# Performance work log

Hardware: AMD Instinct MI355X
Metric: run time of the kernel (lower is better)

## Reference

```python
import jax, jax.numpy as jnp
import numpy as np

B, P, S, D, L = 8, 64, 512, 512, 64


def setup_inputs() -> dict:
    key = jax.random.key(0)
    ks = jax.random.split(key, 12)
    span_repr = jax.random.normal(ks[0], (B, S, D), dtype=jnp.float32)
    predicates = jax.random.randint(ks[1], (B, P), 0, S, dtype=jnp.int64)
    labels = jax.random.randint(ks[2], (B, P, S), 0, L, dtype=jnp.int64)
    long_mask = jnp.ones((B, P, S), dtype=jnp.int64)
    sc = 1.0 / np.sqrt(D)
    # last-layer weights of FFNN linear_p / linear_a (only last layer matters in source)
    Wp = jax.random.normal(ks[3], (D, D), dtype=jnp.float32) * sc
    bp = jnp.zeros((D,), dtype=jnp.float32)
    Wa = jax.random.normal(ks[4], (D, D), dtype=jnp.float32) * sc
    ba = jnp.zeros((D,), dtype=jnp.float32)
    wp = jax.random.normal(ks[5], (D,), dtype=jnp.float32) * sc  # W_p (Linear D->1, no bias)
    wa = jax.random.normal(ks[6], (D,), dtype=jnp.float32) * sc  # W_a
    W1 = jax.random.normal(ks[7], (L, D, D), dtype=jnp.float32) * sc
    W2 = jax.random.normal(ks[8], (2 * D, L), dtype=jnp.float32) * sc
    b = jax.random.normal(ks[9], (1, L), dtype=jnp.float32) * 0.02
    return {"span_repr": span_repr, "predicates": predicates, "labels": labels,
            "long_mask": long_mask, "Wp": Wp, "bp": bp, "Wa": Wa, "ba": ba,
            "wp": wp, "wa": wa, "W1": W1, "W2": W2, "b": b}


def reference(span_repr, predicates, labels, long_mask, Wp, bp, Wa, ba, wp, wa, W1, W2, b):
    d = span_repr.shape[-1]
    # gather predicate representations: [B, P, D]
    pred_repr = jnp.take_along_axis(span_repr, predicates[..., None], axis=1)
    # FFNN (only last layer is effective in source) + scalar projections
    predicates_score = jax.nn.relu(pred_repr @ Wp.T + bp) @ wp        # [B, P]
    argument_score = jax.nn.relu(span_repr @ Wa.T + ba) @ wa          # [B, S]
    p_a_score = predicates_score[:, :, None] + argument_score[:, None, :]  # [B, P, S]
    # biaffine term: matmul(matmul(pred, W1), span^T) -> [B, P, S, L]
    first = jnp.einsum('bpd,lde,bse->bpsl', pred_repr, W1, span_repr)
    # concat(pred, span) @ W2, split to avoid materializing the concat
    second = (jnp.einsum('bpd,dl->bpl', pred_repr, W2[:d])[:, :, None, :]
              + jnp.einsum('bsd,dl->bsl', span_repr, W2[d:])[:, None, :, :])
    combine = first + second + b + p_a_score[..., None]               # [B, P, S, L]
    combine = combine.at[..., -1].set(0.0)
    num_labels = combine.shape[-1]
    # long_mask is all ones, so masked_select is the full flatten
    stack_instance = combine.reshape(-1, num_labels)                  # [B*P*S, L]
    stack_label = labels.reshape(-1)                                  # [B*P*S]
    return stack_instance, stack_label
```

## Files before the change

### kernel.cpp

```cpp
#include <hip/hip_runtime.h>
#include <hip/hip_bf16.h>

typedef __bf16 bf16x8 __attribute__((ext_vector_type(8)));
typedef float f32x4 __attribute__((ext_vector_type(4)));
typedef unsigned short ushort_t;

#define SS 512
#define DD 512
#define LL 64

__device__ __forceinline__ ushort_t f2b(float f) {
    union { float f; unsigned u; } x; x.f = f;
    unsigned r = x.u + 0x7FFFu + ((x.u >> 16) & 1u);
    return (ushort_t)(r >> 16);
}

__device__ __forceinline__ void async16(const void* g, void* l) {
    __builtin_amdgcn_global_load_lds(
        (const __attribute__((address_space(1))) unsigned int*)g,
        (__attribute__((address_space(3))) unsigned int*)l, 16, 0, 0);
}

__device__ __forceinline__ void stage_tile(const ushort_t* __restrict__ A, int lda,
                                           const ushort_t* __restrict__ Bt, int ldb,
                                           int k0, ushort_t* buf) {
    const int t = threadIdx.x;
    const int wbase = (t >> 6) << 10;
#pragma unroll
    for (int p = 0; p < 2; p++) {
        int row = (p << 7) + (t >> 2);
        int kg = (t & 3) ^ ((t >> 3) & 3);
        async16(A + (size_t)row * lda + k0 + kg * 8,
                (char*)buf + (p << 13) + wbase);
        async16(Bt + (size_t)row * ldb + k0 + kg * 8,
                (char*)(buf + 8192) + (p << 13) + wbase);
    }
}

__device__ __forceinline__ void gemm256(const ushort_t* __restrict__ A, int lda,
                                        const ushort_t* __restrict__ Bt, int ldb,
                                        ushort_t* lds, f32x4 (&acc)[8][4]) {
    const int t = threadIdx.x;
    const int lane = t & 63, wid = t >> 6;
    const int wm = wid >> 2, wn = wid & 3;
    const int r15 = lane & 15, kg = lane >> 4;
    const int sx = ((kg ^ ((r15 >> 1) & 3)) << 4);
    const f32x4 z4 = {0.f, 0.f, 0.f, 0.f};
#pragma unroll
    for (int i = 0; i < 8; i++)
#pragma unroll
        for (int j = 0; j < 4; j++) acc[i][j] = z4;

    stage_tile(A, lda, Bt, ldb, 0, lds);
    stage_tile(A, lda, Bt, ldb, 32, lds + 16384);

    for (int T = 0; T < 16; ++T) {
        if (T < 15) asm volatile("s_waitcnt vmcnt(4)" ::: "memory");
        else        asm volatile("s_waitcnt vmcnt(0)" ::: "memory");
        __builtin_amdgcn_s_barrier();
        __builtin_amdgcn_sched_barrier(0);
        const ushort_t* bufA = lds + (T % 3) * 16384;
        const ushort_t* bufB = bufA + 8192;
        const char* pa = (const char*)bufA + (wm * 128 + r15) * 64 + sx;
        const char* pb = (const char*)bufB + (wn * 64 + r15) * 64 + sx;
        bf16x8 af[8], bf[4];
#pragma unroll
        for (int mf = 0; mf < 8; mf++) af[mf] = *(const bf16x8*)(pa + mf * 1024);
#pragma unroll
        for (int nf = 0; nf < 4; nf++) bf[nf] = *(const bf16x8*)(pb + nf * 1024);
        if (T + 2 < 16)
            stage_tile(A, lda, Bt, ldb, (T + 2) * 32, lds + ((T + 2) % 3) * 16384);
#pragma unroll
        for (int mf = 0; mf < 8; mf++)
#pragma unroll
            for (int nf = 0; nf < 4; nf++)
                acc[mf][nf] = __builtin_amdgcn_mfma_f32_16x16x32_bf16(
                    af[mf], bf[nf], acc[mf][nf], 0, 0, 0);
    }
    __syncthreads();
}

__device__ __forceinline__ void stageA2(const ushort_t* __restrict__ A,
                                        int k0, ushort_t* buf) {
    const int t = threadIdx.x;
    const int wbase = (t >> 6) << 10;
#pragma unroll
    for (int p = 0; p < 2; p++) {
        int row = (p << 7) + (t >> 2);
        int kg = (t & 3) ^ ((t >> 3) & 3);
        async16(A + (size_t)row * DD + k0 + kg * 8, (char*)buf + (p << 13) + wbase);
    }
}

__device__ __forceinline__ void gemm256_w1(const ushort_t* __restrict__ predB,
                                           const float* __restrict__ W1le,
                                           ushort_t* lds, f32x4 (&acc)[8][4]) {
    const int t = threadIdx.x;
    const int lane = t & 63, wid = t >> 6;
    const int wm = wid >> 2, wn = wid & 3;
    const int r15 = lane & 15, kg = lane >> 4;
    const int sx = ((kg ^ ((r15 >> 1) & 3)) << 4);
    const f32x4 z4 = {0.f, 0.f, 0.f, 0.f};
#pragma unroll
    for (int i = 0; i < 8; i++)
#pragma unroll
        for (int j = 0; j < 4; j++) acc[i][j] = z4;

    const float* bbase = W1le + (size_t)(kg * 8) * DD + wn * 64 + r15;
    float fb[4][8];
    auto loadB = [&](int k0) {
#pragma unroll
        for (int nf = 0; nf < 4; nf++)
#pragma unroll
            for (int j = 0; j < 8; j++)
                fb[nf][j] = bbase[(size_t)(k0 + j) * DD + nf * 16];
    };

    loadB(0);
    stageA2(predB, 0, lds);
    stageA2(predB, 32, lds + 8192);

    for (int T = 0; T < 16; ++T) {
        if (T < 15) asm volatile("s_waitcnt vmcnt(2)" ::: "memory");
        else        asm volatile("s_waitcnt vmcnt(0)" ::: "memory");
        __builtin_amdgcn_s_barrier();
        __builtin_amdgcn_sched_barrier(0);
        bf16x8 bf[4];
#pragma unroll
        for (int nf = 0; nf < 4; nf++)
#pragma unroll
            for (int j = 0; j < 8; j++) bf[nf][j] = (__bf16)fb[nf][j];
        if (T + 1 < 16) loadB((T + 1) * 32);
        if (T + 2 < 16) stageA2(predB, (T + 2) * 32, lds + ((T + 2) % 3) * 8192);
        const char* pa = (const char*)(lds + (T % 3) * 8192)
                         + (wm * 128 + r15) * 64 + sx;
        bf16x8 af[8];
#pragma unroll
        for (int mf = 0; mf < 8; mf++) af[mf] = *(const bf16x8*)(pa + mf * 1024);
#pragma unroll
        for (int mf = 0; mf < 8; mf++)
#pragma unroll
            for (int nf = 0; nf < 4; nf++)
                acc[mf][nf] = __builtin_amdgcn_mfma_f32_16x16x32_bf16(
                    af[mf], bf[nf], acc[mf][nf], 0, 0, 0);
    }
    __syncthreads();
}

__global__ void __launch_bounds__(512, 2) k_U_small(
    const ushort_t* __restrict__ predB, const float* __restrict__ W1,
    ushort_t* __restrict__ UB,
    const ushort_t* __restrict__ spanB, const ushort_t* __restrict__ WaB,
    const ushort_t* __restrict__ WpB, const ushort_t* __restrict__ W2bT,
    const ushort_t* __restrict__ W2aT,
    const float* __restrict__ ba_, const float* __restrict__ bp_,
    const float* __restrict__ wa, const float* __restrict__ wp,
    float* ascore, float* pscore, float* spanW2, float* predW2) {
    extern __shared__ ushort_t lds[];
    const f32x4 z4 = {0.f, 0.f, 0.f, 0.f};
    const int t = threadIdx.x, lane = t & 63;
    const int r15 = lane & 15, kg = lane >> 4;
    if (blockIdx.x < 256) {
        f32x4 acc[8][4];
        int swz = (blockIdx.x & 7) * 32 + (blockIdx.x >> 3);
        int m0 = (swz & 1) * 256, n0 = (swz >> 1) * 256;
        int l = n0 >> 9, e0 = n0 & 511;
        gemm256_w1(predB + (size_t)m0 * DD, W1 + ((size_t)l * DD) * DD + e0, lds, acc);
        const int wid = t >> 6;
        const int wm = wid >> 2, wn = wid & 3;
        ushort_t* my = lds + wid * 4096;
        int gm = m0 + wm * 128, gn = n0 + wn * 64;
#pragma unroll
        for (int ch = 0; ch < 2; ch++) {
#pragma unroll
            for (int mf2 = 0; mf2 < 4; mf2++)
#pragma unroll
                for (int nf = 0; nf < 4; nf++)
#pragma unroll
                    for (int j = 0; j < 4; j++)
                        my[(mf2 * 16 + kg * 4 + j) * 64 + nf * 16 + r15] =
                            f2b(acc[ch * 4 + mf2][nf][j]);
#pragma unroll
            for (int it = 0; it < 8; it++) {
                int lr = it * 8 + (lane >> 3);
                bf16x8 v = *(const bf16x8*)(my + lr * 64 + (lane & 7) * 8);
                *(bf16x8*)(UB + (size_t)(gm + ch * 64 + lr) * 32768 + gn
                           + (lane & 7) * 8) = v;
            }
        }
        return;
    }
    const bool act = t < 256;
    ushort_t* As = lds;
    ushort_t* Bs = lds + 4096;
    const int wid4 = (t >> 6) & 3;
    const int o0 = wid4 * 1024 + lane * 16;
    int blk = blockIdx.x - 256;
    if (blk < 144) {
        const ushort_t *A, *Bt; const float *bias, *w; float* sc; int m0, n0;
        if (blk < 128) { A = spanB; Bt = WaB; bias = ba_; w = wa; sc = ascore;
                         m0 = (blk >> 2) * 128; n0 = (blk & 3) * 128; }
        else { int q = blk - 128; A = predB; Bt = WpB; bias = bp_; w = wp; sc = pscore;
               m0 = (q >> 2) * 128; n0 = (q & 3) * 128; }
        const ushort_t* Ab = A + (size_t)m0 * DD;
        const ushort_t* Bb = Bt + (size_t)n0 * DD;
        f32x4 acc[4][4];
#pragma unroll
        for (int i = 0; i < 4; i++)
#pragma unroll
            for (int j = 0; j < 4; j++) acc[i][j] = z4;
        int wr = (wid4 >> 1) * 64, wc = (wid4 & 1) * 64;
        for (int k0 = 0; k0 < DD; k0 += 32) {
            if (act) {
#pragma unroll
                for (int p = 0; p < 2; p++) {
                    int o = o0 + p * 4096;
                    async16(Ab + (size_t)(o >> 6) * DD + k0 + ((o & 63) >> 1), (char*)As + o);
                    async16(Bb + (size_t)(o >> 6) * DD + k0 + ((o & 63) >> 1), (char*)Bs + o);
                }
            }
            __syncthreads();
            if (act) {
                bf16x8 af[4], bf[4];
#pragma unroll
                for (int mf = 0; mf < 4; mf++)
                    af[mf] = *(const bf16x8*)(As + (wr + mf * 16 + r15) * 32 + kg * 8);
#pragma unroll
                for (int nf = 0; nf < 4; nf++)
                    bf[nf] = *(const bf16x8*)(Bs + (wc + nf * 16 + r15) * 32 + kg * 8);
#pragma unroll
                for (int mf = 0; mf < 4; mf++)
#pragma unroll
                    for (int nf = 0; nf < 4; nf++)
                        acc[mf][nf] = __builtin_amdgcn_mfma_f32_16x16x32_bf16(
                            af[mf], bf[nf], acc[mf][nf], 0, 0, 0);
            }
            __syncthreads();
        }
        if (act) {
#pragma unroll
            for (int mf = 0; mf < 4; mf++)
#pragma unroll
                for (int j = 0; j < 4; j++) {
                    float v = 0.f;
#pragma unroll
                    for (int nf = 0; nf < 4; nf++) {
                        int col = n0 + wc + nf * 16 + r15;
                        float c = acc[mf][nf][j] + bias[col];
                        if (c > 0.f) v += c * w[col];
                    }
                    v += __shfl_xor(v, 1); v += __shfl_xor(v, 2);
                    v += __shfl_xor(v, 4); v += __shfl_xor(v, 8);
                    if (r15 == 0) atomicAdd(&sc[m0 + wr + mf * 16 + kg * 4 + j], v);
                }
        }
    } else {
        int q = blk - 144;
        const ushort_t *A, *Bt; float* C; int m0;
        if (q < 32) { A = spanB; Bt = W2bT; C = spanW2; m0 = q * 128; }
        else { A = predB; Bt = W2aT; C = predW2; m0 = (q - 32) * 128; }
        const ushort_t* Ab = A + (size_t)m0 * DD;
        f32x4 acc[4][2];
#pragma unroll
        for (int i = 0; i < 4; i++) { acc[i][0] = z4; acc[i][1] = z4; }
        int wr = (wid4 >> 1) * 64, wc = (wid4 & 1) * 32;
        for (int k0 = 0; k0 < DD; k0 += 32) {
            if (act) {
#pragma unroll
                for (int p = 0; p < 2; p++) {
                    int o = o0 + p * 4096;
                    async16(Ab + (size_t)(o >> 6) * DD + k0 + ((o & 63) >> 1), (char*)As + o);
                }
                int o = o0;
                async16(Bt + (size_t)(o >> 6) * DD + k0 + ((o & 63) >> 1), (char*)Bs + o);
            }
            __syncthreads();
            if (act) {
                bf16x8 af[4], bf[2];
#pragma unroll
                for (int mf = 0; mf < 4; mf++)
                    af[mf] = *(const bf16x8*)(As + (wr + mf * 16 + r15) * 32 + kg * 8);
#pragma unroll
                for (int nf = 0; nf < 2; nf++)
                    bf[nf] = *(const bf16x8*)(Bs + (wc + nf * 16 + r15) * 32 + kg * 8);
#pragma unroll
                for (int mf = 0; mf < 4; mf++)
#pragma unroll
                    for (int nf = 0; nf < 2; nf++)
                        acc[mf][nf] = __builtin_amdgcn_mfma_f32_16x16x32_bf16(
                            af[mf], bf[nf], acc[mf][nf], 0, 0, 0);
            }
            __syncthreads();
        }
        if (act) {
#pragma unroll
            for (int mf = 0; mf < 4; mf++)
#pragma unroll
                for (int nf = 0; nf < 2; nf++)
#pragma unroll
                    for (int j = 0; j < 4; j++) {
                        int m = m0 + wr + mf * 16 + kg * 4 + j;
                        int n = wc + nf * 16 + r15;
                        C[(size_t)m * LL + n] = acc[mf][nf][j];
                    }
        }
    }
}

__global__ void __launch_bounds__(512, 2) k_out256(const ushort_t* __restrict__ spanB,
    const ushort_t* __restrict__ UB, const float* __restrict__ spanW2,
    const float* __restrict__ predW2, const float* __restrict__ ascore,
    const float* __restrict__ pscore, const float* __restrict__ bias,
    float* __restrict__ out) {
    extern __shared__ ushort_t lds[];
    f32x4 acc[8][4];
    int swz = (blockIdx.x & 7) * 32 + (blockIdx.x >> 3);
    int b = swz >> 5, r = swz & 31;
    int m0 = (r & 1) * 256, n0 = (r >> 1) * 256;
    gemm256(spanB + ((size_t)b * SS + m0) * DD, DD,
            UB + ((size_t)b * 4096 + n0) * DD, DD, lds, acc);
    const int t = threadIdx.x, lane = t & 63, wid = t >> 6;
    const int wm = wid >> 2, wn = wid & 3, r15 = lane & 15, kg = lane >> 4;
    float cn[4]; int nn[4];
#pragma unroll
    for (int nf = 0; nf < 4; nf++) {
        int n = n0 + wn * 64 + nf * 16 + r15;
        nn[nf] = n;
        cn[nf] = bias[n & 63] + predW2[b * 4096 + n] + pscore[b * 64 + (n >> 6)];
    }
#pragma unroll
    for (int mf = 0; mf < 8; mf++)
#pragma unroll
        for (int j = 0; j < 4; j++) {
            int s = m0 + wm * 128 + mf * 16 + kg * 4 + j;
            float as_ = ascore[b * SS + s];
            const float* sw = spanW2 + ((size_t)b * SS + s) * LL;
#pragma unroll
            for (int nf = 0; nf < 4; nf++) {
                int n = nn[nf], l = n & 63, p = n >> 6;
                float v = acc[mf][nf][j] + cn[nf] + as_ + sw[l];
                if (l == LL - 1) v = 0.f;
                out[(((size_t)b * 64 + p) * SS + s) * LL + l] = v;
            }
        }
}

__global__ __launch_bounds__(256) void k_prep(
    const float* __restrict__ span, const int* __restrict__ preds,
    const int* __restrict__ labels, const float* __restrict__ Wa,
    const float* __restrict__ Wp, const float* __restrict__ W2,
    ushort_t* spanB, ushort_t* predB, ushort_t* WaB, ushort_t* WpB,
    ushort_t* W2aT, ushort_t* W2bT, float* out, float* scores) {
    int blk = blockIdx.x;
    if (blk < 4096) {
        int id = blk * 256 + threadIdx.x;
        if (id < 524288) {
            float4 v = ((const float4*)span)[id];
            ((ushort4*)spanB)[id] = make_ushort4(f2b(v.x), f2b(v.y), f2b(v.z), f2b(v.w));
        } else if (id < 589824) {
            int j = id - 524288;
            int row = j >> 7, c4 = j & 127;
            int b = row >> 6;
            int idx = preds[row];
            float4 v = ((const float4*)(span + ((size_t)(b * SS + idx)) * DD))[c4];
            ((ushort4*)(predB + (size_t)row * DD))[c4] =
                make_ushort4(f2b(v.x), f2b(v.y), f2b(v.z), f2b(v.w));
        } else if (id < 851968) {
            int k = id - 589824;
            out[16777216 + k] = (float)labels[k];
        } else if (id < 917504) {
            int j = id - 851968;
            float4 v = ((const float4*)Wa)[j];
            ((ushort4*)WaB)[j] = make_ushort4(f2b(v.x), f2b(v.y), f2b(v.z), f2b(v.w));
        } else if (id < 983040) {
            int j = id - 917504;
            float4 v = ((const float4*)Wp)[j];
            ((ushort4*)WpB)[j] = make_ushort4(f2b(v.x), f2b(v.y), f2b(v.z), f2b(v.w));
        } else if (id < 1015808) {
            int j = id - 983040;
            W2aT[j] = f2b(W2[(size_t)(j & 511) * LL + (j >> 9)]);
        } else {
            int j = id - 1015808;
            W2bT[j] = f2b(W2[(size_t)((j & 511) + DD) * LL + (j >> 9)]);
        }
    } else {
        int idx = (blk - 4096) * 256 + threadIdx.x;
        if (idx < 4608) scores[idx] = 0.f;
    }
}

extern "C" void kernel_launch(void* const* d_in, const int* in_sizes, int n_in,
                              void* d_out, int out_size, void* d_ws, size_t ws_size,
                              hipStream_t stream) {
    const float* span   = (const float*)d_in[0];
    const int*   preds  = (const int*)d_in[1];
    const int*   labels = (const int*)d_in[2];
    const float* Wp     = (const float*)d_in[4];
    const float* bp_    = (const float*)d_in[5];
    const float* Wa     = (const float*)d_in[6];
    const float* ba_    = (const float*)d_in[7];
    const float* wp     = (const float*)d_in[8];
    const float* wa     = (const float*)d_in[9];
    const float* W1     = (const float*)d_in[10];
    const float* W2     = (const float*)d_in[11];
    const float* bias   = (const float*)d_in[12];
    float* out = (float*)d_out;
    char* ws = (char*)d_ws;

    ushort_t* spanB  = (ushort_t*)(ws + 0);
    ushort_t* predB  = (ushort_t*)(ws + 4194304);
    ushort_t* WaB    = (ushort_t*)(ws + 4718592);
    ushort_t* WpB    = (ushort_t*)(ws + 5242880);
    ushort_t* W2aT   = (ushort_t*)(ws + 5767168);
    ushort_t* W2bT   = (ushort_t*)(ws + 5832704);
    ushort_t* UB     = (ushort_t*)(ws + 39452672);
    float*    ascore = (float*)(ws + 73007104);
    float*    pscore = (float*)(ws + 73023488);
    float*    spanW2 = (float*)(ws + 73025536);
    float*    predW2 = (float*)(ws + 74074112);

    hipFuncSetAttribute((const void*)k_U_small,
                        hipFuncAttributeMaxDynamicSharedMemorySize, 65536);
    hipFuncSetAttribute((const void*)k_out256,
                        hipFuncAttributeMaxDynamicSharedMemorySize, 98304);

    k_prep<<<4114, 256, 0, stream>>>(span, preds, labels, Wa, Wp, W2,
                                     spanB, predB, WaB, WpB, W2aT, W2bT,
                                     out, ascore);

    k_U_small<<<436, 512, 65536, stream>>>(predB, W1, UB,
                                           spanB, WaB, WpB, W2bT, W2aT,
                                           ba_, bp_, wa, wp,
                                           ascore, pscore, spanW2, predW2);

    k_out256<<<256, 512, 98304, stream>>>(spanB, UB, spanW2, predW2,
                                          ascore, pscore, bias, out);
}
```

Measured before the change: 84.26 us.

## Shrink W1 GEMM tiles to 256x128 and schedule small GEMM blocks first

The W1 projection GEMM in k_U_small now uses 256x128 output tiles instead of 256x256, doubling its block count to 512. The grid grows from 436 to 692 blocks and LDS per block drops from 64KB to 48KB. The small score and W2 GEMM blocks move to the front of the grid so they are dispatched first. The aim is better CU load balance and occupancy; the cost is less reuse of the A tile per block and more redundant staging of predB.

```diff
diff --git a/kernel.cpp b/kernel.cpp
--- a/kernel.cpp
+++ b/kernel.cpp
@@ -92,9 +92,9 @@
     }
 }
 
-__device__ __forceinline__ void gemm256_w1(const ushort_t* __restrict__ predB,
-                                           const float* __restrict__ W1le,
-                                           ushort_t* lds, f32x4 (&acc)[8][4]) {
+__device__ __forceinline__ void gemm256x128_w1(const ushort_t* __restrict__ predB,
+                                               const float* __restrict__ W1le,
+                                               ushort_t* lds, f32x4 (&acc)[8][2]) {
     const int t = threadIdx.x;
     const int lane = t & 63, wid = t >> 6;
     const int wm = wid >> 2, wn = wid & 3;
@@ -102,15 +102,13 @@
     const int sx = ((kg ^ ((r15 >> 1) & 3)) << 4);
     const f32x4 z4 = {0.f, 0.f, 0.f, 0.f};
 #pragma unroll
-    for (int i = 0; i < 8; i++)
-#pragma unroll
-        for (int j = 0; j < 4; j++) acc[i][j] = z4;
-
-    const float* bbase = W1le + (size_t)(kg * 8) * DD + wn * 64 + r15;
-    float fb[4][8];
+    for (int i = 0; i < 8; i++) { acc[i][0] = z4; acc[i][1] = z4; }
+
+    const float* bbase = W1le + (size_t)(kg * 8) * DD + wn * 32 + r15;
+    float fb[2][8];
     auto loadB = [&](int k0) {
 #pragma unroll
-        for (int nf = 0; nf < 4; nf++)
+        for (int nf = 0; nf < 2; nf++)
 #pragma unroll
             for (int j = 0; j < 8; j++)
                 fb[nf][j] = bbase[(size_t)(k0 + j) * DD + nf * 16];
@@ -125,9 +123,9 @@
         else        asm volatile("s_waitcnt vmcnt(0)" ::: "memory");
         __builtin_amdgcn_s_barrier();
         __builtin_amdgcn_sched_barrier(0);
-        bf16x8 bf[4];
-#pragma unroll
-        for (int nf = 0; nf < 4; nf++)
+        bf16x8 bf[2];
+#pragma unroll
+        for (int nf = 0; nf < 2; nf++)
 #pragma unroll
             for (int j = 0; j < 8; j++) bf[nf][j] = (__bf16)fb[nf][j];
         if (T + 1 < 16) loadB((T + 1) * 32);
@@ -140,7 +138,7 @@
 #pragma unroll
         for (int mf = 0; mf < 8; mf++)
 #pragma unroll
-            for (int nf = 0; nf < 4; nf++)
+            for (int nf = 0; nf < 2; nf++)
                 acc[mf][nf] = __builtin_amdgcn_mfma_f32_16x16x32_bf16(
                     af[mf], bf[nf], acc[mf][nf], 0, 0, 0);
     }
@@ -160,32 +158,36 @@
     const f32x4 z4 = {0.f, 0.f, 0.f, 0.f};
     const int t = threadIdx.x, lane = t & 63;
     const int r15 = lane & 15, kg = lane >> 4;
-    if (blockIdx.x < 256) {
-        f32x4 acc[8][4];
-        int swz = (blockIdx.x & 7) * 32 + (blockIdx.x >> 3);
-        int m0 = (swz & 1) * 256, n0 = (swz >> 1) * 256;
-        int l = n0 >> 9, e0 = n0 & 511;
-        gemm256_w1(predB + (size_t)m0 * DD, W1 + ((size_t)l * DD) * DD + e0, lds, acc);
+    if (blockIdx.x >= 180) {
+        f32x4 acc[8][2];
+        int u = blockIdx.x - 180;
+        int swz = (u & 7) * 64 + (u >> 3);
+        int m0 = (swz & 1) * 256;
+        int nidx = swz >> 1;
+        int n0 = nidx * 128;
+        int l = nidx >> 2, e0 = (nidx & 3) * 128;
+        gemm256x128_w1(predB + (size_t)m0 * DD,
+                       W1 + (size_t)l * DD * DD + e0, lds, acc);
         const int wid = t >> 6;
         const int wm = wid >> 2, wn = wid & 3;
-        ushort_t* my = lds + wid * 4096;
-        int gm = m0 + wm * 128, gn = n0 + wn * 64;
+        ushort_t* my = lds + wid * 2048;
+        int gm = m0 + wm * 128, gn = n0 + wn * 32;
 #pragma unroll
         for (int ch = 0; ch < 2; ch++) {
 #pragma unroll
             for (int mf2 = 0; mf2 < 4; mf2++)
 #pragma unroll
-                for (int nf = 0; nf < 4; nf++)
+                for (int nf = 0; nf < 2; nf++)
 #pragma unroll
                     for (int j = 0; j < 4; j++)
-                        my[(mf2 * 16 + kg * 4 + j) * 64 + nf * 16 + r15] =
+                        my[(mf2 * 16 + kg * 4 + j) * 32 + nf * 16 + r15] =
                             f2b(acc[ch * 4 + mf2][nf][j]);
 #pragma unroll
-            for (int it = 0; it < 8; it++) {
-                int lr = it * 8 + (lane >> 3);
-                bf16x8 v = *(const bf16x8*)(my + lr * 64 + (lane & 7) * 8);
-                *(bf16x8*)(UB + (size_t)(gm + ch * 64 + lr) * 32768 + gn
-                           + (lane & 7) * 8) = v;
+            for (int pass = 0; pass < 4; pass++) {
+                int row = pass * 16 + (lane >> 2);
+                bf16x8 v = *(const bf16x8*)(my + row * 32 + (lane & 3) * 8);
+                *(bf16x8*)(UB + (size_t)(gm + ch * 64 + row) * 32768 + gn
+                           + (lane & 3) * 8) = v;
             }
         }
         return;
@@ -195,7 +197,7 @@
     ushort_t* Bs = lds + 4096;
     const int wid4 = (t >> 6) & 3;
     const int o0 = wid4 * 1024 + lane * 16;
-    int blk = blockIdx.x - 256;
+    int blk = blockIdx.x;
     if (blk < 144) {
         const ushort_t *A, *Bt; const float *bias, *w; float* sc; int m0, n0;
         if (blk < 128) { A = spanB; Bt = WaB; bias = ba_; w = wa; sc = ascore;
@@ -420,7 +422,7 @@
     float*    predW2 = (float*)(ws + 74074112);
 
     hipFuncSetAttribute((const void*)k_U_small,
-                        hipFuncAttributeMaxDynamicSharedMemorySize, 65536);
+                        hipFuncAttributeMaxDynamicSharedMemorySize, 49152);
     hipFuncSetAttribute((const void*)k_out256,
                         hipFuncAttributeMaxDynamicSharedMemorySize, 98304);
 
@@ -428,7 +430,7 @@
                                      spanB, predB, WaB, WpB, W2aT, W2bT,
                                      out, ascore);
 
-    k_U_small<<<436, 512, 65536, stream>>>(predB, W1, UB,
+    k_U_small<<<692, 512, 49152, stream>>>(predB, W1, UB,
                                            spanB, WaB, WpB, W2bT, W2aT,
                                            ba_, bp_, wa, wp,
                                            ascore, pscore, spanW2, predW2);
```

New measurement: 77.43 us (median of 2 runs). 1.09x faster.

## Stage fp32 W1 tiles through LDS with async loads in U GEMM

Applied to the files above, without the earlier changes.

The W1 operand of the large U GEMM is no longer loaded straight from global memory into registers with strided scalar loads. It is now staged as fp32 tiles into swizzled LDS with async global-to-LDS copies, triple-buffered alongside the A tiles, then read from LDS and converted to bf16. Small GEMM blocks are moved to the front of the grid so they dispatch first. The LDS footprint grows to 144KB, which forces one block per CU (launch bounds change from 2 to 1) and reduces occupancy.

```diff
diff --git a/kernel.cpp b/kernel.cpp
--- a/kernel.cpp
+++ b/kernel.cpp
@@ -92,9 +92,22 @@
     }
 }
 
-__device__ __forceinline__ void gemm256_w1(const ushort_t* __restrict__ predB,
-                                           const float* __restrict__ W1le,
-                                           ushort_t* lds, f32x4 (&acc)[8][4]) {
+__device__ __forceinline__ void stageB_w1(const float* __restrict__ W1le,
+                                          int k0, ushort_t* buf) {
+    const int t = threadIdx.x;
+#pragma unroll
+    for (int p = 0; p < 4; p++) {
+        int o = p * 8192 + t * 16;
+        int row = o >> 10;
+        int c = (o >> 4) & 63;
+        int sc = (c + 2 * ((row >> 3) & 3)) & 63;
+        async16(W1le + (size_t)(k0 + row) * DD + sc * 4, (char*)buf + o);
+    }
+}
+
+__device__ __forceinline__ void gemm256_w1lds(const ushort_t* __restrict__ predB,
+                                              const float* __restrict__ W1le,
+                                              ushort_t* lds, f32x4 (&acc)[8][4]) {
     const int t = threadIdx.x;
     const int lane = t & 63, wid = t >> 6;
     const int wm = wid >> 2, wn = wid & 3;
@@ -106,33 +119,37 @@
 #pragma unroll
         for (int j = 0; j < 4; j++) acc[i][j] = z4;
 
-    const float* bbase = W1le + (size_t)(kg * 8) * DD + wn * 64 + r15;
-    float fb[4][8];
-    auto loadB = [&](int k0) {
-#pragma unroll
-        for (int nf = 0; nf < 4; nf++)
-#pragma unroll
-            for (int j = 0; j < 8; j++)
-                fb[nf][j] = bbase[(size_t)(k0 + j) * DD + nf * 16];
-    };
-
-    loadB(0);
-    stageA2(predB, 0, lds);
-    stageA2(predB, 32, lds + 8192);
+    ushort_t* Ab = lds;
+    ushort_t* Bb = lds + 24576;
+
+    stageB_w1(W1le, 0, Bb);
+    stageA2(predB, 0, Ab);
+    stageB_w1(W1le, 32, Bb + 16384);
+    stageA2(predB, 32, Ab + 8192);
 
     for (int T = 0; T < 16; ++T) {
-        if (T < 15) asm volatile("s_waitcnt vmcnt(2)" ::: "memory");
+        if (T < 15) asm volatile("s_waitcnt vmcnt(6)" ::: "memory");
         else        asm volatile("s_waitcnt vmcnt(0)" ::: "memory");
         __builtin_amdgcn_s_barrier();
         __builtin_amdgcn_sched_barrier(0);
+        const char* bF = (const char*)(Bb + (T % 3) * 16384);
         bf16x8 bf[4];
 #pragma unroll
-        for (int nf = 0; nf < 4; nf++)
-#pragma unroll
-            for (int j = 0; j < 8; j++) bf[nf][j] = (__bf16)fb[nf][j];
-        if (T + 1 < 16) loadB((T + 1) * 32);
-        if (T + 2 < 16) stageA2(predB, (T + 2) * 32, lds + ((T + 2) % 3) * 8192);
-        const char* pa = (const char*)(lds + (T % 3) * 8192)
+        for (int nf = 0; nf < 4; nf++) {
+            int ebase = wn * 16 + nf * 4 + (r15 >> 2);
+#pragma unroll
+            for (int j = 0; j < 8; j++) {
+                int chunk = (ebase - 2 * kg) & 63;
+                float v = *(const float*)(bF + (size_t)(kg * 8 + j) * 1024
+                                          + (chunk << 4) + (r15 & 3) * 4);
+                bf[nf][j] = (__bf16)v;
+            }
+        }
+        if (T + 2 < 16) {
+            stageB_w1(W1le, (T + 2) * 32, Bb + ((T + 2) % 3) * 16384);
+            stageA2(predB, (T + 2) * 32, Ab + ((T + 2) % 3) * 8192);
+        }
+        const char* pa = (const char*)(Ab + (T % 3) * 8192)
                          + (wm * 128 + r15) * 64 + sx;
         bf16x8 af[8];
 #pragma unroll
@@ -147,7 +164,7 @@
     __syncthreads();
 }
 
-__global__ void __launch_bounds__(512, 2) k_U_small(
+__global__ void __launch_bounds__(512, 1) k_U_small(
     const ushort_t* __restrict__ predB, const float* __restrict__ W1,
     ushort_t* __restrict__ UB,
     const ushort_t* __restrict__ spanB, const ushort_t* __restrict__ WaB,
@@ -160,12 +177,14 @@
     const f32x4 z4 = {0.f, 0.f, 0.f, 0.f};
     const int t = threadIdx.x, lane = t & 63;
     const int r15 = lane & 15, kg = lane >> 4;
-    if (blockIdx.x < 256) {
+    if (blockIdx.x >= 180) {
         f32x4 acc[8][4];
-        int swz = (blockIdx.x & 7) * 32 + (blockIdx.x >> 3);
+        int u = blockIdx.x - 180;
+        int swz = (u & 7) * 32 + (u >> 3);
         int m0 = (swz & 1) * 256, n0 = (swz >> 1) * 256;
         int l = n0 >> 9, e0 = n0 & 511;
-        gemm256_w1(predB + (size_t)m0 * DD, W1 + ((size_t)l * DD) * DD + e0, lds, acc);
+        gemm256_w1lds(predB + (size_t)m0 * DD,
+                      W1 + ((size_t)l * DD) * DD + e0, lds, acc);
         const int wid = t >> 6;
         const int wm = wid >> 2, wn = wid & 3;
         ushort_t* my = lds + wid * 4096;
@@ -187,6 +206,7 @@
                 *(bf16x8*)(UB + (size_t)(gm + ch * 64 + lr) * 32768 + gn
                            + (lane & 7) * 8) = v;
             }
+            __syncthreads();
         }
         return;
     }
@@ -195,15 +215,15 @@
     ushort_t* Bs = lds + 4096;
     const int wid4 = (t >> 6) & 3;
     const int o0 = wid4 * 1024 + lane * 16;
-    int blk = blockIdx.x - 256;
+    int blk = blockIdx.x;
     if (blk < 144) {
         const ushort_t *A, *Bt; const float *bias, *w; float* sc; int m0, n0;
         if (blk < 128) { A = spanB; Bt = WaB; bias = ba_; w = wa; sc = ascore;
                          m0 = (blk >> 2) * 128; n0 = (blk & 3) * 128; }
         else { int q = blk - 128; A = predB; Bt = WpB; bias = bp_; w = wp; sc = pscore;
                m0 = (q >> 2) * 128; n0 = (q & 3) * 128; }
-        const ushort_t* Ab = A + (size_t)m0 * DD;
-        const ushort_t* Bb = Bt + (size_t)n0 * DD;
+        const ushort_t* Ab2 = A + (size_t)m0 * DD;
+        const ushort_t* Bb2 = Bt + (size_t)n0 * DD;
         f32x4 acc[4][4];
 #pragma unroll
         for (int i = 0; i < 4; i++)
@@ -215,8 +235,8 @@
 #pragma unroll
                 for (int p = 0; p < 2; p++) {
                     int o = o0 + p * 4096;
-                    async16(Ab + (size_t)(o >> 6) * DD + k0 + ((o & 63) >> 1), (char*)As + o);
-                    async16(Bb + (size_t)(o >> 6) * DD + k0 + ((o & 63) >> 1), (char*)Bs + o);
+                    async16(Ab2 + (size_t)(o >> 6) * DD + k0 + ((o & 63) >> 1), (char*)As + o);
+                    async16(Bb2 + (size_t)(o >> 6) * DD + k0 + ((o & 63) >> 1), (char*)Bs + o);
                 }
             }
             __syncthreads();
@@ -259,7 +279,7 @@
         const ushort_t *A, *Bt; float* C; int m0;
         if (q < 32) { A = spanB; Bt = W2bT; C = spanW2; m0 = q * 128; }
         else { A = predB; Bt = W2aT; C = predW2; m0 = (q - 32) * 128; }
-        const ushort_t* Ab = A + (size_t)m0 * DD;
+        const ushort_t* Ab2 = A + (size_t)m0 * DD;
         f32x4 acc[4][2];
 #pragma unroll
         for (int i = 0; i < 4; i++) { acc[i][0] = z4; acc[i][1] = z4; }
@@ -269,7 +289,7 @@
 #pragma unroll
                 for (int p = 0; p < 2; p++) {
                     int o = o0 + p * 4096;
-                    async16(Ab + (size_t)(o >> 6) * DD + k0 + ((o & 63) >> 1), (char*)As + o);
+                    async16(Ab2 + (size_t)(o >> 6) * DD + k0 + ((o & 63) >> 1), (char*)As + o);
                 }
                 int o = o0;
                 async16(Bt + (size_t)(o >> 6) * DD + k0 + ((o & 63) >> 1), (char*)Bs + o);
@@ -420,7 +440,7 @@
     float*    predW2 = (float*)(ws + 74074112);
 
     hipFuncSetAttribute((const void*)k_U_small,
-                        hipFuncAttributeMaxDynamicSharedMemorySize, 65536);
+                        hipFuncAttributeMaxDynamicSharedMemorySize, 147456);
     hipFuncSetAttribute((const void*)k_out256,
                         hipFuncAttributeMaxDynamicSharedMemorySize, 98304);
 
@@ -428,10 +448,10 @@
                                      spanB, predB, WaB, WpB, W2aT, W2bT,
                                      out, ascore);
 
-    k_U_small<<<436, 512, 65536, stream>>>(predB, W1, UB,
-                                           spanB, WaB, WpB, W2bT, W2aT,
-                                           ba_, bp_, wa, wp,
-                                           ascore, pscore, spanW2, predW2);
+    k_U_small<<<436, 512, 147456, stream>>>(predB, W1, UB,
+                                            spanB, WaB, WpB, W2bT, W2aT,
+                                            ba_, bp_, wa, wp,
+                                            ascore, pscore, spanW2, predW2);
 
     k_out256<<<256, 512, 98304, stream>>>(spanB, UB, spanW2, predW2,
                                           ascore, pscore, bias, out);
```

Measured after the change: 83.20 us. About the same (-1.3%).
